# Performance work log

Measured on AMD Instinct MI355X. Metric: run time of the kernel, lower is better.

The kernel has to match this reference:

```python
import jax
import jax.numpy as jnp
from jax import lax
import numpy as np

B, CIN, COUT, RANK, K, H, W = 16, 256, 256, 64, 3, 112, 112
PAD = 1


def setup_inputs() -> dict:
    key = jax.random.key(0)
    k1, k2, k3, k4, k5 = jax.random.split(key, 5)
    x = jax.random.normal(k1, (B, CIN, H, W), dtype=jnp.float32)
    # head: `rank` stacked 1x1 conv weights, each [COUT, CIN]
    w_head = jax.random.normal(k2, (RANK, COUT, CIN), dtype=jnp.float32) * 0.05
    # body: Conv2d(COUT -> RANK, kernel (K,1)), OIHW layout
    w_body = jax.random.normal(k3, (RANK, COUT, K, 1), dtype=jnp.float32) * 0.05
    # tail: Conv2d(RANK -> COUT, kernel (1,K)), OIHW layout, with bias
    w_tail = jax.random.normal(k4, (COUT, RANK, 1, K), dtype=jnp.float32) * 0.05
    b_tail = jax.random.normal(k5, (COUT,), dtype=jnp.float32) * 0.05
    return {"x": x, "w_head": w_head, "w_body": w_body, "w_tail": w_tail, "b_tail": b_tail}


_DN = lax.conv_dimension_numbers((B, CIN, H, W), (COUT, CIN, 1, 1), ("NCHW", "OIHW", "NCHW"))


def reference(x, w_head, w_body, w_tail, b_tail):
    # Sum of rank 1x1 convs over the same input == one 1x1 conv with summed
    # weights (conv is linear in the weight) — same math, one pass.
    w_sum = w_head.sum(axis=0)                      # [COUT, CIN]
    y = jnp.einsum("bihw,oi->bohw", x, w_sum)       # [B, COUT, H, W]
    # body: (K,1) conv, stride (1,1), padding (PAD, 0)
    y = lax.conv_general_dilated(y, w_body, window_strides=(1, 1),
                                 padding=((PAD, PAD), (0, 0)),
                                 dimension_numbers=_DN)  # [B, RANK, H, W]
    # tail: (1,K) conv, stride (1,1), padding (0, PAD), plus bias
    y = lax.conv_general_dilated(y, w_tail, window_strides=(1, 1),
                                 padding=((0, 0), (PAD, PAD)),
                                 dimension_numbers=_DN)  # [B, COUT, H, W]
    return y + b_tail[None, :, None, None]
```

## Files before the change

### kernel.cpp

```cpp
#include <hip/hip_runtime.h>
#include <stdint.h>

#define CIN 256
#define COUT 256
#define RANK 64
#define H_ 112
#define W_ 112
#define HW_ (112*112)

typedef unsigned short ushort_t;
typedef short bf16x8 __attribute__((ext_vector_type(8)));
typedef float f32x4 __attribute__((ext_vector_type(4)));

__device__ __forceinline__ unsigned rne2(float a, float b){
  unsigned ua = __builtin_bit_cast(unsigned, a);
  unsigned ub = __builtin_bit_cast(unsigned, b);
  ua += 0x7FFFu + ((ua >> 16) & 1u);
  ub += 0x7FFFu + ((ub >> 16) & 1u);
  return (ua >> 16) | (ub & 0xFFFF0000u);
}
__device__ __forceinline__ unsigned short rne1(float a){
  unsigned ua = __builtin_bit_cast(unsigned, a);
  ua += 0x7FFFu + ((ua >> 16) & 1u);
  return (unsigned short)(ua >> 16);
}

__global__ __launch_bounds__(256) void k_wsum(const float* __restrict__ wh,
                                              float* __restrict__ wsum){
  int o = blockIdx.x, i = threadIdx.x;
  float s = 0.f;
  for (int k = 0; k < RANK; ++k) s += wh[(k*COUT + o)*CIN + i];
  wsum[o*CIN + i] = s;
}

__global__ __launch_bounds__(256) void k_weff(const float* __restrict__ wb,
                                              const float* __restrict__ wsum,
                                              unsigned short* __restrict__ weff){
  int bid = blockIdx.x;
  int dh = bid >> 6, r = bid & 63;
  int i = threadIdx.x;
  float s = 0.f;
  for (int o = 0; o < COUT; ++o)
    s += wb[(r*COUT + o)*3 + dh] * wsum[o*CIN + i];
  weff[bid*CIN + i] = rne1(s);
}

__global__ __launch_bounds__(256) void k_wtp(const float* __restrict__ wt,
                                             unsigned short* __restrict__ wtp){
  int o = blockIdx.x, t = threadIdx.x;
  if (t < 192){
    int dw = t >> 6, r = t & 63;
    wtp[o*192 + t] = rne1(wt[(o*RANK + r)*3 + dw]);
  }
}

__global__ __launch_bounds__(256) void k_xt(const float* __restrict__ x,
                                            unsigned short* __restrict__ xt){
  __shared__ float ldsf[64*120];
  const int tid = threadIdx.x;
  const int bb = blockIdx.x / 114, hh = blockIdx.x % 114;
  const int h = hh - 1;
  unsigned short* dst = xt + ((size_t)(bb*114 + hh))*28672;

  if (h < 0 || h >= H_){
    uint4 z = {0,0,0,0};
    #pragma unroll
    for (int j = 0; j < 14; ++j)
      *(uint4*)(dst + (tid + 256*j)*8) = z;
    return;
  }

  for (int i0p = 0; i0p < 4; ++i0p){
    int c = tid / 28, wq = tid % 28;
    #pragma unroll
    for (int j = 0; j < 7; ++j){
      const float4 v = *(const float4*)(x + ((size_t)(bb*CIN + i0p*64 + c))*HW_ + h*W_ + wq*4);
      *(float4*)&ldsf[c*120 + wq*4] = v;
      wq += 4; c += 9; if (wq >= 28){ wq -= 28; c += 1; }
    }
    __syncthreads();
    for (int chunk = tid; chunk < 896; chunk += 256){
      int g8 = chunk / 112, w = chunk % 112;
      const float* src = &ldsf[(g8*8)*120 + w];
      uint4 st;
      st.x = rne2(src[0],     src[120]);
      st.y = rne2(src[240],   src[360]);
      st.z = rne2(src[480],   src[600]);
      st.w = rne2(src[720],   src[840]);
      *(uint4*)(dst + (size_t)(i0p*896 + chunk)*8) = st;
    }
    __syncthreads();
  }
}

__global__ __launch_bounds__(256,2) void k_body(const unsigned short* __restrict__ xt,
                                                const unsigned short* __restrict__ weff,
                                                unsigned short* __restrict__ y2){
  __shared__ alignas(16) unsigned short lds[2*4*3584];
  const int tid  = threadIdx.x;
  const int wid  = tid >> 6, lane = tid & 63, g = lane >> 4, l15 = lane & 15;
  const int bb   = blockIdx.x / 56, hb = blockIdx.x % 56;
  const int h0   = hb*2;
  const int hloc = wid >> 1, rhalf = wid & 1;

  f32x4 acc[2][7];
  #pragma unroll
  for (int a = 0; a < 2; ++a)
    #pragma unroll
    for (int b = 0; b < 7; ++b) acc[a][b] = (f32x4){0.f,0.f,0.f,0.f};

  const unsigned short* rowbase = xt + ((size_t)(bb*114 + h0 + wid)*8)*3584;

  auto stage = [&](unsigned short* dstbuf, int i0){
    const unsigned short* src = rowbase + (size_t)i0*3584 + lane*8;
    unsigned short* dstb = dstbuf + wid*3584;
    #pragma unroll
    for (int k = 0; k < 7; ++k)
      __builtin_amdgcn_global_load_lds(
        (const __attribute__((address_space(1))) void*)(src + k*512),
        (__attribute__((address_space(3))) void*)(dstb + k*512), 16, 0, 0);
  };

  auto compute = [&](const unsigned short* buf, int i0){
    #pragma unroll
    for (int dh = 0; dh < 3; ++dh){
      const int row = hloc + dh;
      const unsigned short* ab = weff + (size_t)(dh*64 + rhalf*32 + l15)*CIN + i0*32 + g*8;
      bf16x8 af0 = *(const bf16x8*)(ab);
      bf16x8 af1 = *(const bf16x8*)(ab + 16*CIN);
      const unsigned short* qb = buf + row*3584 + g*896 + l15*8;
      #pragma unroll
      for (int wt = 0; wt < 7; ++wt){
        bf16x8 bfv = *(const bf16x8*)(qb + wt*128);
        acc[0][wt] = __builtin_amdgcn_mfma_f32_16x16x32_bf16(af0, bfv, acc[0][wt], 0, 0, 0);
        acc[1][wt] = __builtin_amdgcn_mfma_f32_16x16x32_bf16(af1, bfv, acc[1][wt], 0, 0, 0);
      }
    }
  };

  unsigned short* cur = lds;
  unsigned short* nxt = lds + 14336;
  stage(cur, 0);
  __syncthreads();
  for (int t = 0; t < 8; ++t){
    if (t < 7) stage(nxt, t+1);
    compute(cur, t);
    __syncthreads();
    unsigned short* tmp = cur; cur = nxt; nxt = tmp;
  }

  const int h = h0 + hloc;
  unsigned short* yb = y2 + ((size_t)(bb*H_ + h)*W_)*64;
  #pragma unroll
  for (int wt = 0; wt < 7; ++wt){
    #pragma unroll
    for (int rt = 0; rt < 2; ++rt){
      unsigned lo = rne2(acc[rt][wt][0], acc[rt][wt][1]);
      unsigned hi = rne2(acc[rt][wt][2], acc[rt][wt][3]);
      uint2 st; st.x = lo; st.y = hi;
      *(uint2*)(yb + (wt*16 + l15)*64 + rhalf*32 + rt*16 + g*4) = st;
    }
  }
}

__global__ __launch_bounds__(256,2) void k_tail(const unsigned short* __restrict__ y2,
                                                const unsigned short* __restrict__ wtp,
                                                const float* __restrict__ bias,
                                                float* __restrict__ out){
  __shared__ alignas(16) unsigned short ldsY[114*72];
  const int tid = threadIdx.x;
  const int wid = tid >> 6, lane = tid & 63, g = lane >> 4, l15 = lane & 15;
  const int bb  = blockIdx.x / 112, h = blockIdx.x % 112;
  const unsigned short* yb = y2 + ((size_t)(bb*H_ + h)*W_)*64;

  for (int idx = tid; idx < 114*8; idx += 256){
    int w = idx >> 3, c = idx & 7;
    uint4 v = {0,0,0,0};
    if (w >= 1 && w <= 112) v = *(const uint4*)(yb + (w-1)*64 + c*8);
    *(uint4*)&ldsY[w*72 + c*8] = v;
  }
  __syncthreads();

  f32x4 acc[4][7];
  #pragma unroll
  for (int a = 0; a < 4; ++a)
    #pragma unroll
    for (int b = 0; b < 7; ++b) acc[a][b] = (f32x4){0.f,0.f,0.f,0.f};

  #pragma unroll
  for (int s = 0; s < 6; ++s){
    bf16x8 af[4];
    const int abase = (wid*64 + l15)*192 + s*32 + g*8;
    #pragma unroll
    for (int rt = 0; rt < 4; ++rt)
      af[rt] = *(const bf16x8*)(wtp + abase + rt*16*192);
    const unsigned short* qb = ldsY + (l15 + (s>>1))*72 + (s&1)*32 + g*8;
    #pragma unroll
    for (int wt = 0; wt < 7; ++wt){
      bf16x8 bf = *(const bf16x8*)(qb + wt*16*72);
      #pragma unroll
      for (int rt = 0; rt < 4; ++rt)
        acc[rt][wt] = __builtin_amdgcn_mfma_f32_16x16x32_bf16(af[rt], bf, acc[rt][wt], 0, 0, 0);
    }
  }

  float bv[4][4];
  #pragma unroll
  for (int rt = 0; rt < 4; ++rt)
    #pragma unroll
    for (int ii = 0; ii < 4; ++ii)
      bv[rt][ii] = bias[wid*64 + rt*16 + g*4 + ii];

  float* ob = out + ((size_t)bb*COUT)*HW_ + h*W_;
  #pragma unroll
  for (int rt = 0; rt < 4; ++rt)
    #pragma unroll
    for (int wt = 0; wt < 7; ++wt)
      #pragma unroll
      for (int ii = 0; ii < 4; ++ii)
        ob[(size_t)(wid*64 + rt*16 + g*4 + ii)*HW_ + wt*16 + l15] = acc[rt][wt][ii] + bv[rt][ii];
}

extern "C" void kernel_launch(void* const* d_in, const int* in_sizes, int n_in,
                              void* d_out, int out_size, void* d_ws, size_t ws_size,
                              hipStream_t stream) {
  const float* x      = (const float*)d_in[0];
  const float* w_head = (const float*)d_in[1];
  const float* w_body = (const float*)d_in[2];
  const float* w_tail = (const float*)d_in[3];
  const float* b_tail = (const float*)d_in[4];
  float* out = (float*)d_out;

  char* ws = (char*)d_ws;
  unsigned short* y2   = (unsigned short*)ws;
  float*          wsum = (float*)(ws + 25690112);
  unsigned short* weff = (unsigned short*)(ws + 25952256);
  unsigned short* wtp  = (unsigned short*)(ws + 26050560);

  unsigned short* xt = (unsigned short*)d_out;

  k_wsum<<<256, 256, 0, stream>>>(w_head, wsum);
  k_weff<<<192, 256, 0, stream>>>(w_body, wsum, weff);
  k_wtp <<<256, 256, 0, stream>>>(w_tail, wtp);
  k_xt  <<<16*114, 256, 0, stream>>>(x, xt);
  k_body<<<16*56, 256, 0, stream>>>(xt, weff, y2);
  k_tail<<<16*112, 256, 0, stream>>>(y2, wtp, b_tail, out);
}
```

Measured before the change: 197.9 us.

## Fuse body and tail convs via LDS, merge weight prep kernels, chunk batches

The body (K,1) conv and tail (1,K) conv now run in one kernel. The bf16 intermediate stays in LDS with zero-padded width borders instead of making a round trip through global memory. The weight-sum work folds into the x-transpose kernel as extra blocks, and the weight-eff and tail-weight packing merge into one launch, which cuts the launch count. The transposed input moves from the output buffer into the workspace and is processed in batch chunks sized to the available workspace. That could add launches when the workspace is small, and the fused kernel does the tail MFMA work in two serial passes per wave.

```diff
diff --git a/kernel.cpp b/kernel.cpp
--- a/kernel.cpp
+++ b/kernel.cpp
@@ -8,7 +8,6 @@
 #define W_ 112
 #define HW_ (112*112)
 
-typedef unsigned short ushort_t;
 typedef short bf16x8 __attribute__((ext_vector_type(8)));
 typedef float f32x4 __attribute__((ext_vector_type(4)));
 
@@ -25,42 +24,24 @@
   return (unsigned short)(ua >> 16);
 }
 
-__global__ __launch_bounds__(256) void k_wsum(const float* __restrict__ wh,
-                                              float* __restrict__ wsum){
-  int o = blockIdx.x, i = threadIdx.x;
-  float s = 0.f;
-  for (int k = 0; k < RANK; ++k) s += wh[(k*COUT + o)*CIN + i];
-  wsum[o*CIN + i] = s;
-}
-
-__global__ __launch_bounds__(256) void k_weff(const float* __restrict__ wb,
-                                              const float* __restrict__ wsum,
-                                              unsigned short* __restrict__ weff){
-  int bid = blockIdx.x;
-  int dh = bid >> 6, r = bid & 63;
-  int i = threadIdx.x;
-  float s = 0.f;
-  for (int o = 0; o < COUT; ++o)
-    s += wb[(r*COUT + o)*3 + dh] * wsum[o*CIN + i];
-  weff[bid*CIN + i] = rne1(s);
-}
-
-__global__ __launch_bounds__(256) void k_wtp(const float* __restrict__ wt,
-                                             unsigned short* __restrict__ wtp){
-  int o = blockIdx.x, t = threadIdx.x;
-  if (t < 192){
-    int dw = t >> 6, r = t & 63;
-    wtp[o*192 + t] = rne1(wt[(o*RANK + r)*3 + dw]);
-  }
-}
-
-__global__ __launch_bounds__(256) void k_xt(const float* __restrict__ x,
-                                            unsigned short* __restrict__ xt){
+__global__ __launch_bounds__(256) void k_pre1(const float* __restrict__ x,
+                                              unsigned short* __restrict__ xt,
+                                              const float* __restrict__ wh,
+                                              float* __restrict__ wsum,
+                                              int base_b, int nb){
   __shared__ float ldsf[64*120];
   const int tid = threadIdx.x;
-  const int bb = blockIdx.x / 114, hh = blockIdx.x % 114;
+  if (blockIdx.x >= (unsigned)(nb*114)){
+    int o = blockIdx.x - nb*114;
+    float s = 0.f;
+    for (int k = 0; k < RANK; ++k) s += wh[(k*COUT + o)*CIN + tid];
+    wsum[o*CIN + tid] = s;
+    return;
+  }
+  const int lb = blockIdx.x / 114, hh = blockIdx.x % 114;
+  const int bb = base_b + lb;
   const int h = hh - 1;
-  unsigned short* dst = xt + ((size_t)(bb*114 + hh))*28672;
+  unsigned short* dst = xt + ((size_t)(lb*114 + hh))*28672;
 
   if (h < 0 || h >= H_){
     uint4 z = {0,0,0,0};
@@ -79,27 +60,53 @@
       wq += 4; c += 9; if (wq >= 28){ wq -= 28; c += 1; }
     }
     __syncthreads();
-    for (int chunk = tid; chunk < 896; chunk += 256){
-      int g8 = chunk / 112, w = chunk % 112;
+    for (int ck = tid; ck < 896; ck += 256){
+      int g8 = ck / 112, w = ck % 112;
       const float* src = &ldsf[(g8*8)*120 + w];
       uint4 st;
       st.x = rne2(src[0],     src[120]);
       st.y = rne2(src[240],   src[360]);
       st.z = rne2(src[480],   src[600]);
       st.w = rne2(src[720],   src[840]);
-      *(uint4*)(dst + (size_t)(i0p*896 + chunk)*8) = st;
+      *(uint4*)(dst + (size_t)(i0p*896 + ck)*8) = st;
     }
     __syncthreads();
   }
 }
 
-__global__ __launch_bounds__(256,2) void k_body(const unsigned short* __restrict__ xt,
-                                                const unsigned short* __restrict__ weff,
-                                                unsigned short* __restrict__ y2){
-  __shared__ alignas(16) unsigned short lds[2*4*3584];
+__global__ __launch_bounds__(256) void k_pre2(const float* __restrict__ wb,
+                                              const float* __restrict__ wsum,
+                                              unsigned short* __restrict__ weff,
+                                              const float* __restrict__ wt,
+                                              unsigned short* __restrict__ wtp){
+  const int tid = threadIdx.x;
+  if (blockIdx.x < 192){
+    int bid = blockIdx.x;
+    int dh = bid >> 6, r = bid & 63;
+    float s = 0.f;
+    for (int o = 0; o < COUT; ++o)
+      s += wb[(r*COUT + o)*3 + dh] * wsum[o*CIN + tid];
+    weff[bid*CIN + tid] = rne1(s);
+  } else {
+    int o = blockIdx.x - 192;
+    if (tid < 192){
+      int dw = tid >> 6, r = tid & 63;
+      wtp[o*192 + tid] = rne1(wt[(o*RANK + r)*3 + dw]);
+    }
+  }
+}
+
+__global__ __launch_bounds__(256,2) void k_fused(const unsigned short* __restrict__ xt,
+                                                 const unsigned short* __restrict__ weff,
+                                                 const unsigned short* __restrict__ wtp,
+                                                 const float* __restrict__ bias,
+                                                 float* __restrict__ out,
+                                                 int base_b){
+  __shared__ alignas(16) unsigned short lds[28672];
   const int tid  = threadIdx.x;
   const int wid  = tid >> 6, lane = tid & 63, g = lane >> 4, l15 = lane & 15;
-  const int bb   = blockIdx.x / 56, hb = blockIdx.x % 56;
+  const int lb   = blockIdx.x / 56, hb = blockIdx.x % 56;
+  const int bb   = base_b + lb;
   const int h0   = hb*2;
   const int hloc = wid >> 1, rhalf = wid & 1;
 
@@ -109,7 +116,7 @@
     #pragma unroll
     for (int b = 0; b < 7; ++b) acc[a][b] = (f32x4){0.f,0.f,0.f,0.f};
 
-  const unsigned short* rowbase = xt + ((size_t)(bb*114 + h0 + wid)*8)*3584;
+  const unsigned short* rowbase = xt + ((size_t)(lb*114 + h0 + wid)*8)*3584;
 
   auto stage = [&](unsigned short* dstbuf, int i0){
     const unsigned short* src = rowbase + (size_t)i0*3584 + lane*8;
@@ -149,8 +156,11 @@
     unsigned short* tmp = cur; cur = nxt; nxt = tmp;
   }
 
-  const int h = h0 + hloc;
-  unsigned short* yb = y2 + ((size_t)(bb*H_ + h)*W_)*64;
+  unsigned short* y2b = lds;
+  if (tid < 32){
+    int hh = tid >> 4, wsel = (tid >> 3) & 1, rq = tid & 7;
+    *(uint4*)(y2b + hh*8208 + (wsel ? 113 : 0)*72 + rq*8) = (uint4){0,0,0,0};
+  }
   #pragma unroll
   for (int wt = 0; wt < 7; ++wt){
     #pragma unroll
@@ -158,67 +168,50 @@
       unsigned lo = rne2(acc[rt][wt][0], acc[rt][wt][1]);
       unsigned hi = rne2(acc[rt][wt][2], acc[rt][wt][3]);
       uint2 st; st.x = lo; st.y = hi;
-      *(uint2*)(yb + (wt*16 + l15)*64 + rhalf*32 + rt*16 + g*4) = st;
-    }
-  }
-}
-
-__global__ __launch_bounds__(256,2) void k_tail(const unsigned short* __restrict__ y2,
-                                                const unsigned short* __restrict__ wtp,
-                                                const float* __restrict__ bias,
-                                                float* __restrict__ out){
-  __shared__ alignas(16) unsigned short ldsY[114*72];
-  const int tid = threadIdx.x;
-  const int wid = tid >> 6, lane = tid & 63, g = lane >> 4, l15 = lane & 15;
-  const int bb  = blockIdx.x / 112, h = blockIdx.x % 112;
-  const unsigned short* yb = y2 + ((size_t)(bb*H_ + h)*W_)*64;
-
-  for (int idx = tid; idx < 114*8; idx += 256){
-    int w = idx >> 3, c = idx & 7;
-    uint4 v = {0,0,0,0};
-    if (w >= 1 && w <= 112) v = *(const uint4*)(yb + (w-1)*64 + c*8);
-    *(uint4*)&ldsY[w*72 + c*8] = v;
+      *(uint2*)(y2b + hloc*8208 + (wt*16 + l15 + 1)*72 + rhalf*32 + rt*16 + g*4) = st;
+    }
   }
   __syncthreads();
 
-  f32x4 acc[4][7];
+  const int h = h0 + hloc;
   #pragma unroll
-  for (int a = 0; a < 4; ++a)
-    #pragma unroll
-    for (int b = 0; b < 7; ++b) acc[a][b] = (f32x4){0.f,0.f,0.f,0.f};
-
-  #pragma unroll
-  for (int s = 0; s < 6; ++s){
-    bf16x8 af[4];
-    const int abase = (wid*64 + l15)*192 + s*32 + g*8;
-    #pragma unroll
-    for (int rt = 0; rt < 4; ++rt)
-      af[rt] = *(const bf16x8*)(wtp + abase + rt*16*192);
-    const unsigned short* qb = ldsY + (l15 + (s>>1))*72 + (s&1)*32 + g*8;
-    #pragma unroll
-    for (int wt = 0; wt < 7; ++wt){
-      bf16x8 bf = *(const bf16x8*)(qb + wt*16*72);
+  for (int opass = 0; opass < 2; ++opass){
+    const int obase = rhalf*128 + opass*64;
+    f32x4 a2[4][7];
+    #pragma unroll
+    for (int a = 0; a < 4; ++a)
+      #pragma unroll
+      for (int b = 0; b < 7; ++b) a2[a][b] = (f32x4){0.f,0.f,0.f,0.f};
+
+    #pragma unroll
+    for (int s = 0; s < 6; ++s){
+      bf16x8 af[4];
+      const unsigned short* ab = wtp + (size_t)(obase + l15)*192 + s*32 + g*8;
       #pragma unroll
       for (int rt = 0; rt < 4; ++rt)
-        acc[rt][wt] = __builtin_amdgcn_mfma_f32_16x16x32_bf16(af[rt], bf, acc[rt][wt], 0, 0, 0);
-    }
-  }
-
-  float bv[4][4];
-  #pragma unroll
-  for (int rt = 0; rt < 4; ++rt)
-    #pragma unroll
-    for (int ii = 0; ii < 4; ++ii)
-      bv[rt][ii] = bias[wid*64 + rt*16 + g*4 + ii];
-
-  float* ob = out + ((size_t)bb*COUT)*HW_ + h*W_;
-  #pragma unroll
-  for (int rt = 0; rt < 4; ++rt)
-    #pragma unroll
-    for (int wt = 0; wt < 7; ++wt)
-      #pragma unroll
-      for (int ii = 0; ii < 4; ++ii)
-        ob[(size_t)(wid*64 + rt*16 + g*4 + ii)*HW_ + wt*16 + l15] = acc[rt][wt][ii] + bv[rt][ii];
+        af[rt] = *(const bf16x8*)(ab + rt*16*192);
+      const unsigned short* qb = y2b + hloc*8208 + (l15 + (s >> 1))*72 + (s & 1)*32 + g*8;
+      #pragma unroll
+      for (int wt = 0; wt < 7; ++wt){
+        bf16x8 bv = *(const bf16x8*)(qb + wt*16*72);
+        #pragma unroll
+        for (int rt = 0; rt < 4; ++rt)
+          a2[rt][wt] = __builtin_amdgcn_mfma_f32_16x16x32_bf16(af[rt], bv, a2[rt][wt], 0, 0, 0);
+      }
+    }
+
+    float* ob = out + ((size_t)(bb*COUT) + obase)*HW_ + h*W_;
+    #pragma unroll
+    for (int rt = 0; rt < 4; ++rt){
+      #pragma unroll
+      for (int ii = 0; ii < 4; ++ii){
+        float bvv = bias[obase + rt*16 + g*4 + ii];
+        #pragma unroll
+        for (int wt = 0; wt < 7; ++wt)
+          ob[(size_t)(rt*16 + g*4 + ii)*HW_ + wt*16 + l15] = a2[rt][wt][ii] + bvv;
+      }
+    }
+  }
 }
 
 extern "C" void kernel_launch(void* const* d_in, const int* in_sizes, int n_in,
@@ -230,19 +223,29 @@
   const float* w_tail = (const float*)d_in[3];
   const float* b_tail = (const float*)d_in[4];
   float* out = (float*)d_out;
-
   char* ws = (char*)d_ws;
-  unsigned short* y2   = (unsigned short*)ws;
-  float*          wsum = (float*)(ws + 25690112);
-  unsigned short* weff = (unsigned short*)(ws + 25952256);
-  unsigned short* wtp  = (unsigned short*)(ws + 26050560);
-
-  unsigned short* xt = (unsigned short*)d_out;
-
-  k_wsum<<<256, 256, 0, stream>>>(w_head, wsum);
-  k_weff<<<192, 256, 0, stream>>>(w_body, wsum, weff);
-  k_wtp <<<256, 256, 0, stream>>>(w_tail, wtp);
-  k_xt  <<<16*114, 256, 0, stream>>>(x, xt);
-  k_body<<<16*56, 256, 0, stream>>>(xt, weff, y2);
-  k_tail<<<16*112, 256, 0, stream>>>(y2, wtp, b_tail, out);
-}
+
+  float*          wsum = (float*)ws;
+  unsigned short* weff = (unsigned short*)(ws + 262144);
+  unsigned short* wtp  = (unsigned short*)(ws + 360448);
+  unsigned short* xt   = (unsigned short*)(ws + 458752);
+
+  const size_t XT_ROW_BYTES = 57344;
+  const size_t XT_PER_B     = 114 * XT_ROW_BYTES;
+  size_t avail = (ws_size > 458752) ? ws_size - 458752 : 0;
+  int chunk_b = (int)(avail / XT_PER_B);
+  if (chunk_b > 16) chunk_b = 16;
+  if (chunk_b < 1)  chunk_b = 1;
+  int nchunks = (16 + chunk_b - 1) / chunk_b;
+
+  int base = 0;
+  for (int c = 0; c < nchunks; ++c){
+    int remaining = 16 - base;
+    int nb = (remaining + (nchunks - c) - 1) / (nchunks - c);
+    k_pre1<<<nb*114 + (c == 0 ? 256 : 0), 256, 0, stream>>>(x, xt, w_head, wsum, base, nb);
+    if (c == 0)
+      k_pre2<<<448, 256, 0, stream>>>(w_body, wsum, weff, w_tail, wtp);
+    k_fused<<<nb*56, 256, 0, stream>>>(xt, weff, wtp, b_tail, out, base);
+    base += nb;
+  }
+}
```

Measured after the change: 181.6 us. -8.3%, faster.
